# Performance work log

Measured on AMD Instinct MI355X. Metric: run time of the kernel, lower is better.

## Reference

```python
import jax, jax.numpy as jnp
import numpy as np

N_USERS = 100000
N_ITEMS = 50000
D = 64
N_LAYERS = 3
E_RAW = 2_000_000
B = 4096


def setup_inputs() -> dict:
    rng = np.random.RandomState(0)
    u = rng.randint(0, N_USERS, E_RAW).astype(np.int64)
    i = rng.randint(0, N_ITEMS, E_RAW).astype(np.int64)
    lin = np.unique(u * N_ITEMS + i)  # dedupe interactions like the dok_matrix would
    u = (lin // N_ITEMS).astype(np.int32)
    i = (lin % N_ITEMS).astype(np.int32)
    deg_u = np.bincount(u, minlength=N_USERS).astype(np.float64)
    deg_i = np.bincount(i, minlength=N_ITEMS).astype(np.float64)
    inv_u = np.where(deg_u > 0, 1.0 / np.sqrt(np.maximum(deg_u, 1.0)), 0.0)
    inv_i = np.where(deg_i > 0, 1.0 / np.sqrt(np.maximum(deg_i, 1.0)), 0.0)
    val = (inv_u[u] * inv_i[i]).astype(np.float32)  # D^-1/2 A D^-1/2 entries
    # symmetric bipartite Laplacian: user block rows then item block rows
    rows = np.concatenate([u, i + N_USERS]).astype(np.int32)
    cols = np.concatenate([i + N_USERS, u]).astype(np.int32)
    vals = np.concatenate([val, val])

    key = jax.random.key(0)
    k1, k2, k3, k4 = jax.random.split(key, 4)
    embeds = jax.random.normal(k1, (N_USERS + N_ITEMS, D), jnp.float32) * 0.1
    users = jax.random.randint(k2, (B,), 0, N_USERS)
    pos_items = jax.random.randint(k3, (B,), 0, N_ITEMS)
    neg_items = jax.random.randint(k4, (B,), 0, N_ITEMS)
    return dict(embeds=embeds, vals=jnp.asarray(vals), rows=jnp.asarray(rows),
                cols=jnp.asarray(cols), users=users, pos_items=pos_items,
                neg_items=neg_items)


def reference(embeds, vals, rows, cols, users, pos_items, neg_items):
    N = N_USERS + N_ITEMS
    cur = embeds
    acc = embeds  # running sum over layer embeddings (incl. layer 0)
    for _ in range(N_LAYERS):
        msg = vals[:, None] * cur[cols]                      # [nnz, D] gather
        cur = jax.ops.segment_sum(msg, rows, num_segments=N)  # SpMM scatter-add
        acc = acc + cur
    mean = acc / (N_LAYERS + 1)
    user_e = mean[:N_USERS]
    item_e = mean[N_USERS:]
    return user_e[users], item_e[pos_items], item_e[neg_items]
```

## Files before the change

kernel.cpp:

```cpp
#include <hip/hip_runtime.h>
#include <hip/hip_bf16.h>

#define N_USERS 100000
#define N_ITEMS 50000
#define N_TOT   150000
#define D       64
#define NBUCK   ((N_ITEMS + 255) >> 8)
#define BCAP    12288
#define CONVU_B 391
#define FLAG_B  48
#define SCAT_K  32

typedef float v2f __attribute__((ext_vector_type(2)));

__device__ __forceinline__ unsigned bf16rn(float f) {
    unsigned x = __float_as_uint(f);
    return (x + 0x7FFFu + ((x >> 16) & 1u)) >> 16;
}
__device__ __forceinline__ unsigned packbf(float a, float b) {
    return bf16rn(a) | (bf16rn(b) << 16);
}
__device__ __forceinline__ int lower_bound(const int* __restrict__ a, int n, int key) {
    int lo = 0, hi = n;
    while (lo < hi) {
        int mid = (lo + hi) >> 1;
        if (a[mid] < key) lo = mid + 1; else hi = mid;
    }
    return lo;
}

__global__ __launch_bounds__(256) void preA_kernel(
        const float* __restrict__ embeds, const int* __restrict__ rows,
        const int* __restrict__ cols, int* __restrict__ user_ptr,
        unsigned* __restrict__ ebfS, float* __restrict__ invrow,
        const int* __restrict__ users, const int* __restrict__ pos,
        const int* __restrict__ neg, unsigned char* __restrict__ flags,
        int* __restrict__ ccur, int* __restrict__ tmp,
        unsigned short* __restrict__ cols16, int E, int B) {
    int b = blockIdx.x, t = threadIdx.x;
    if (b < CONVU_B) {
        __shared__ int ptr_s[257];
        __shared__ float inv_s[256];
        int base = b * 256;
        int r = base + t;
        int v = lower_bound(rows, E, r);
        ptr_s[t] = v;
        if (r <= N_USERS) user_ptr[r] = v;
        if (t == 0) ptr_s[256] = lower_bound(rows, E, base + 256);
        __syncthreads();
        if (r < N_USERS) {
            int deg = ptr_s[t + 1] - ptr_s[t];
            float inv = (deg > 0) ? (float)(1.0 / sqrt((double)deg)) : 0.f;
            inv_s[t] = inv;
            invrow[r] = inv;
        } else inv_s[t] = 0.f;
        __syncthreads();
        int fl = t & 15;
        #pragma unroll
        for (int i = 0; i < 16; ++i) {
            int lr = i * 16 + (t >> 4);
            int row = base + lr;
            if (row < N_USERS) {
                float inv = inv_s[lr];
                float4 v4 = *(const float4*)(embeds + (size_t)row * D + fl * 4);
                uint2 o;
                o.x = packbf(inv * v4.x, inv * v4.y);
                o.y = packbf(inv * v4.z, inv * v4.w);
                *(uint2*)(ebfS + (size_t)row * 32 + fl * 2) = o;
            }
        }
    } else if (b < CONVU_B + FLAG_B) {
        int k = (b - CONVU_B) * 256 + t;
        if (k < 3 * B) {
            int row;
            if (k < B)          row = users[k];
            else if (k < 2 * B) row = N_USERS + pos[k - B];
            else                row = N_USERS + neg[k - 2 * B];
            flags[row] = 1;
        }
    } else {
        __shared__ int ebuf[256 * SCAT_K];
        __shared__ unsigned char bbuf[256 * SCAT_K];
        __shared__ int cnt[NBUCK];
        __shared__ int basep[NBUCK];
        int chunk = (b - CONVU_B - FLAG_B) * (256 * SCAT_K);
        if (t < NBUCK) cnt[t] = 0;
        __syncthreads();
        #pragma unroll 8
        for (int k = 0; k < SCAT_K; ++k) {
            int e = chunk + k * 256 + t;
            int idx = k * 256 + t;
            if (e < E) {
                int i = cols[e] - N_USERS;
                cols16[e] = (unsigned short)i;
                int bu = i >> 8;
                ebuf[idx] = ((i & 255) << 17) | rows[e];
                bbuf[idx] = (unsigned char)bu;
                atomicAdd(&cnt[bu], 1);
            } else bbuf[idx] = 255;
        }
        __syncthreads();
        if (t < NBUCK) {
            int c = cnt[t];
            basep[t] = c ? atomicAdd(&ccur[t], c) : 0;
            cnt[t] = 0;
        }
        __syncthreads();
        #pragma unroll 4
        for (int k = 0; k < SCAT_K; ++k) {
            int idx = k * 256 + t;
            int bu = bbuf[idx];
            if (bu < NBUCK) {
                int pos2 = basep[bu] + atomicAdd(&cnt[bu], 1);
                if (pos2 < BCAP)
                    tmp[(size_t)bu * BCAP + pos2] = ebuf[idx];
            }
        }
    }
}

__global__ __launch_bounds__(256) void preB_kernel(
        const int* __restrict__ tmp, const int* __restrict__ ccur,
        const float* __restrict__ embeds,
        int* __restrict__ item_beg, int* __restrict__ item_end,
        int* __restrict__ nbr, unsigned* __restrict__ ebfS,
        unsigned* __restrict__ bb1, float* __restrict__ invrow) {
    int b = blockIdx.x, t = threadIdx.x;
    if (b == NBUCK) {
        if (t < 16) {
            *(uint2*)(ebfS + (size_t)N_TOT * 32 + t * 2) = make_uint2(0u, 0u);
            *(uint2*)(bb1  + (size_t)N_TOT * 32 + t * 2) = make_uint2(0u, 0u);
        }
        if (t == 0) invrow[N_TOT] = 0.f;
        return;
    }
    __shared__ int stage[BCAP];
    __shared__ int hist[256];
    __shared__ int scn[256];
    __shared__ int curs[256];
    __shared__ float inv_s[256];
    int n = ccur[b]; if (n > BCAP) n = BCAP;
    const int* src = tmp + (size_t)b * BCAP;
    hist[t] = 0;
    __syncthreads();
    int n4 = n >> 2;
    const int4* src4 = (const int4*)src;
    for (int p = t; p < n4; p += 256) {
        int4 q = src4[p];
        *(int4*)(stage + p * 4) = q;
        atomicAdd(&hist[q.x >> 17], 1);
        atomicAdd(&hist[q.y >> 17], 1);
        atomicAdd(&hist[q.z >> 17], 1);
        atomicAdd(&hist[q.w >> 17], 1);
    }
    for (int p = (n4 << 2) + t; p < n; p += 256) {
        int q = src[p];
        stage[p] = q;
        atomicAdd(&hist[q >> 17], 1);
    }
    __syncthreads();
    scn[t] = hist[t];
    __syncthreads();
    for (int off = 1; off < 256; off <<= 1) {
        int x = (t >= off) ? scn[t - off] : 0;
        __syncthreads();
        scn[t] += x;
        __syncthreads();
    }
    {
        int excl = scn[t] - hist[t];
        curs[t] = excl;
        int gi = (b << 8) + t;
        float inv = (hist[t] > 0) ? (float)(1.0 / sqrt((double)hist[t])) : 0.f;
        inv_s[t] = inv;
        if (gi < N_ITEMS) {
            item_beg[gi] = b * BCAP + excl;
            item_end[gi] = b * BCAP + excl + hist[t];
            invrow[N_USERS + gi] = inv;
        }
    }
    __syncthreads();
    int* dst = nbr + (size_t)b * BCAP;
    for (int p = t; p < n4; p += 256) {
        int4 q = *(const int4*)(stage + p * 4);
        int p0 = atomicAdd(&curs[q.x >> 17], 1); dst[p0] = q.x & 0x1FFFF;
        int p1 = atomicAdd(&curs[q.y >> 17], 1); dst[p1] = q.y & 0x1FFFF;
        int p2 = atomicAdd(&curs[q.z >> 17], 1); dst[p2] = q.z & 0x1FFFF;
        int p3 = atomicAdd(&curs[q.w >> 17], 1); dst[p3] = q.w & 0x1FFFF;
    }
    for (int p = (n4 << 2) + t; p < n; p += 256) {
        int q = stage[p];
        int pos = atomicAdd(&curs[q >> 17], 1);
        dst[pos] = q & 0x1FFFF;
    }
    int fl = t & 15;
    #pragma unroll
    for (int i = 0; i < 16; ++i) {
        int lr = i * 16 + (t >> 4);
        int gi = (b << 8) + lr;
        if (gi < N_ITEMS) {
            int row = N_USERS + gi;
            float inv = inv_s[lr];
            float4 v4 = *(const float4*)(embeds + (size_t)row * D + fl * 4);
            uint2 o;
            o.x = packbf(inv * v4.x, inv * v4.y);
            o.y = packbf(inv * v4.z, inv * v4.w);
            *(uint2*)(ebfS + (size_t)row * 32 + fl * 2) = o;
        }
    }
}

__global__ __launch_bounds__(256) void agg_kernel(
        const unsigned* __restrict__ gsrc,
        float* __restrict__ nxt, unsigned* __restrict__ nxtb,
        const float* __restrict__ invrow,
        const unsigned char* __restrict__ flags,
        const int* __restrict__ user_ptr, const unsigned short* __restrict__ cols16,
        const int* __restrict__ item_beg, const int* __restrict__ item_end,
        const int* __restrict__ nbr) {
    int wave = (int)((blockIdx.x * blockDim.x + threadIdx.x) >> 6);
    int lane = (int)(threadIdx.x & 63);
    if (wave >= (N_TOT >> 2)) return;
    int r  = lane >> 4;
    int q  = lane & 15;
    int g2 = q >> 3;
    int fl = q & 7;

    int row = (wave << 2) + r;
    bool is_user = row < N_USERS;
    int s, epos, dummy;
    const unsigned* sb;
    if (is_user) {
        s = user_ptr[row]; epos = user_ptr[row + 1];
        sb = gsrc + (size_t)N_USERS * 32; dummy = N_ITEMS;
    } else {
        int i = row - N_USERS; s = item_beg[i]; epos = item_end[i];
        sb = gsrc; dummy = N_TOT;
    }
    int deg = epos - s;
    int mdeg = deg;
    mdeg = max(mdeg, __shfl_xor(mdeg, 16));
    mdeg = max(mdeg, __shfl_xor(mdeg, 32));
    int nchunk = (mdeg + 15) >> 4;

    v2f a0 = {0.f, 0.f}, a1 = {0.f, 0.f}, a2 = {0.f, 0.f}, a3 = {0.f, 0.f};

    for (int ch = 0; ch < nchunk; ++ch) {
        int base = s + (ch << 4);
        int cnt = epos - base;
        if (cnt > 16) cnt = 16;
        int col = dummy;
        if (q < cnt)
            col = is_user ? (int)cols16[base + q] : nbr[base + q];
        int cm = mdeg - (ch << 4); if (cm > 16) cm = 16;
        int tcm = (cm + 1) >> 1;
        #pragma unroll 8
        for (int t = 0; t < tcm; ++t) {
            int c = __shfl(col, (r << 4) + 2 * t + g2);
            uint4 qv = *(const uint4*)(sb + (size_t)c * 32 + fl * 4);
            v2f p0 = {__uint_as_float(qv.x << 16), __uint_as_float(qv.x & 0xFFFF0000u)};
            v2f p1 = {__uint_as_float(qv.y << 16), __uint_as_float(qv.y & 0xFFFF0000u)};
            v2f p2 = {__uint_as_float(qv.z << 16), __uint_as_float(qv.z & 0xFFFF0000u)};
            v2f p3 = {__uint_as_float(qv.w << 16), __uint_as_float(qv.w & 0xFFFF0000u)};
            a0 += p0; a1 += p1; a2 += p2; a3 += p3;
        }
    }
    float acc[8] = {a0.x, a0.y, a1.x, a1.y, a2.x, a2.y, a3.x, a3.y};
    #pragma unroll
    for (int j = 0; j < 8; ++j)
        acc[j] += __shfl_xor(acc[j], 8);
    if (q < 8) {
        float inv = invrow[row];
        float f[8];
        #pragma unroll
        for (int j = 0; j < 8; ++j) f[j] = inv * acc[j];
        uint4 o;
        o.x = packbf(inv * f[0], inv * f[1]); o.y = packbf(inv * f[2], inv * f[3]);
        o.z = packbf(inv * f[4], inv * f[5]); o.w = packbf(inv * f[6], inv * f[7]);
        *(uint4*)(nxtb + (size_t)row * 32 + fl * 4) = o;
        if (flags[row]) {
            size_t ro = (size_t)row * D + fl * 8;
            *(float4*)(nxt + ro)     = make_float4(f[0], f[1], f[2], f[3]);
            *(float4*)(nxt + ro + 4) = make_float4(f[4], f[5], f[6], f[7]);
        }
    }
}

__global__ __launch_bounds__(256) void agg3_fused_kernel(
        const unsigned* __restrict__ gsrc,
        const float* __restrict__ e0, const float* __restrict__ e1,
        const float* __restrict__ e2, const float* __restrict__ invrow,
        const int* __restrict__ users, const int* __restrict__ pos,
        const int* __restrict__ neg,
        const int* __restrict__ user_ptr, const unsigned short* __restrict__ cols16,
        const int* __restrict__ item_beg, const int* __restrict__ item_end,
        const int* __restrict__ nbr,
        float* __restrict__ out, int B) {
    int slot = (int)((blockIdx.x * blockDim.x + threadIdx.x) >> 6);
    int lane = (int)(threadIdx.x & 63);
    if (slot >= 3 * B) return;
    int g  = lane >> 3;
    int fl = lane & 7;

    int row;
    if (slot < B)          row = users[slot];
    else if (slot < 2 * B) row = N_USERS + pos[slot - B];
    else                   row = N_USERS + neg[slot - 2 * B];

    bool is_user = row < N_USERS;
    int s, epos, dummy;
    const unsigned* sb;
    if (is_user) {
        s = user_ptr[row]; epos = user_ptr[row + 1];
        sb = gsrc + (size_t)N_USERS * 32; dummy = N_ITEMS;
    } else {
        int i = row - N_USERS; s = item_beg[i]; epos = item_end[i];
        sb = gsrc; dummy = N_TOT;
    }

    v2f a0 = {0.f, 0.f}, a1 = {0.f, 0.f}, a2 = {0.f, 0.f}, a3 = {0.f, 0.f};

    for (int base = s; base < epos; base += 64) {
        int cnt = epos - base; if (cnt > 64) cnt = 64;
        int col = dummy;
        if (lane < cnt)
            col = is_user ? (int)cols16[base + lane] : nbr[base + lane];
        int tcount = (cnt + 7) >> 3;
        #pragma unroll 8
        for (int t = 0; t < tcount; ++t) {
            int c = __shfl(col, 8 * t + g);
            uint4 q = *(const uint4*)(sb + (size_t)c * 32 + fl * 4);
            v2f p0 = {__uint_as_float(q.x << 16), __uint_as_float(q.x & 0xFFFF0000u)};
            v2f p1 = {__uint_as_float(q.y << 16), __uint_as_float(q.y & 0xFFFF0000u)};
            v2f p2 = {__uint_as_float(q.z << 16), __uint_as_float(q.z & 0xFFFF0000u)};
            v2f p3 = {__uint_as_float(q.w << 16), __uint_as_float(q.w & 0xFFFF0000u)};
            a0 += p0; a1 += p1; a2 += p2; a3 += p3;
        }
    }
    float acc[8] = {a0.x, a0.y, a1.x, a1.y, a2.x, a2.y, a3.x, a3.y};
    #pragma unroll
    for (int j = 0; j < 8; ++j) {
        acc[j] += __shfl_xor(acc[j], 8);
        acc[j] += __shfl_xor(acc[j], 16);
        acc[j] += __shfl_xor(acc[j], 32);
    }
    if (lane < 8) {
        float inv = invrow[row];
        size_t ro = (size_t)row * D + fl * 8;
        float4 x0 = *(const float4*)(e0 + ro), x1 = *(const float4*)(e0 + ro + 4);
        float4 y0 = *(const float4*)(e1 + ro), y1 = *(const float4*)(e1 + ro + 4);
        float4 z0 = *(const float4*)(e2 + ro), z1 = *(const float4*)(e2 + ro + 4);
        float4 r0, r1;
        r0.x = (x0.x + y0.x + z0.x + inv * acc[0]) * 0.25f;
        r0.y = (x0.y + y0.y + z0.y + inv * acc[1]) * 0.25f;
        r0.z = (x0.z + y0.z + z0.z + inv * acc[2]) * 0.25f;
        r0.w = (x0.w + y0.w + z0.w + inv * acc[3]) * 0.25f;
        r1.x = (x1.x + y1.x + z1.x + inv * acc[4]) * 0.25f;
        r1.y = (x1.y + y1.y + z1.y + inv * acc[5]) * 0.25f;
        r1.z = (x1.z + y1.z + z1.z + inv * acc[6]) * 0.25f;
        r1.w = (x1.w + y1.w + z1.w + inv * acc[7]) * 0.25f;
        size_t oo = (size_t)slot * D + fl * 8;
        *(float4*)(out + oo)     = r0;
        *(float4*)(out + oo + 4) = r1;
    }
}

extern "C" void kernel_launch(void* const* d_in, const int* in_sizes, int n_in,
                              void* d_out, int out_size, void* d_ws, size_t ws_size,
                              hipStream_t stream) {
    const float* embeds = (const float*)d_in[0];
    const int*   rows   = (const int*)d_in[2];
    const int*   cols   = (const int*)d_in[3];
    const int*   users  = (const int*)d_in[4];
    const int*   pos    = (const int*)d_in[5];
    const int*   neg    = (const int*)d_in[6];
    const int E2 = in_sizes[1];
    const int E  = E2 / 2;
    const int B  = in_sizes[4];

    char* ws = (char*)d_ws;
    size_t off = 0;
    auto alloc = [&](size_t bytes) { void* p = ws + off; off = (off + bytes + 255) & ~(size_t)255; return p; };
    float*    buf1     = (float*)   alloc((size_t)N_TOT * D * sizeof(float));
    float*    buf2     = (float*)   alloc((size_t)N_TOT * D * sizeof(float));
    unsigned* ebfS     = (unsigned*)alloc((size_t)(N_TOT + 1) * 32 * sizeof(unsigned));
    unsigned* bb1      = (unsigned*)alloc((size_t)(N_TOT + 1) * 32 * sizeof(unsigned));
    int*      nbr      = (int*)     alloc((size_t)NBUCK * BCAP * sizeof(int));
    unsigned short* cols16 = (unsigned short*)alloc((size_t)E * sizeof(unsigned short));
    int*      user_ptr = (int*)     alloc((size_t)(N_USERS + 1) * sizeof(int));
    int*      item_beg = (int*)     alloc((size_t)N_ITEMS * sizeof(int));
    int*      item_end = (int*)     alloc((size_t)N_ITEMS * sizeof(int));
    float*    invrow   = (float*)   alloc((size_t)(N_TOT + 1) * sizeof(float));
    int*      ccur     = (int*)     alloc((size_t)NBUCK * sizeof(int));
    unsigned char* flags = (unsigned char*)alloc((size_t)N_TOT);
    int*      tmp      = (int*)buf1;

    size_t zspan = ((char*)flags + N_TOT) - (char*)ccur;
    hipMemsetAsync(ccur, 0, zspan, stream);
    const int scatB = (E + 256 * SCAT_K - 1) / (256 * SCAT_K);
    preA_kernel<<<CONVU_B + FLAG_B + scatB, 256, 0, stream>>>(
        embeds, rows, cols, user_ptr, ebfS, invrow, users, pos, neg, flags,
        ccur, tmp, cols16, E, B);
    preB_kernel<<<NBUCK + 1, 256, 0, stream>>>(
        tmp, ccur, embeds, item_beg, item_end, nbr, ebfS, bb1, invrow);

    const int blocks = N_TOT / 16;
    agg_kernel<<<blocks, 256, 0, stream>>>(ebfS, buf1, bb1, invrow, flags, user_ptr,
                                           cols16, item_beg, item_end, nbr);
    agg_kernel<<<blocks, 256, 0, stream>>>(bb1, buf2, ebfS, invrow, flags, user_ptr,
                                           cols16, item_beg, item_end, nbr);

    agg3_fused_kernel<<<(3 * B + 3) / 4, 256, 0, stream>>>(
        ebfS, embeds, buf1, buf2, invrow, users, pos, neg,
        user_ptr, cols16, item_beg, item_end, nbr, (float*)d_out, B);
}
```

Baseline: 292.6 us.

## Build user CSR pointers from row boundaries during scatter instead of binary search

Replaces the per-user binary search over the sorted rows array with boundary detection in the edge-scatter pass: each edge compares its row with the next and writes user_ptr for the users in between. The user-degree normalisation and bf16 conversion of user embeddings move into extra blocks of the second preprocessing kernel, which now reads the finished user_ptr. This removes about 100k log(E) dependent global-memory searches, at the cost of an extra adjacent load per edge and loop-based pointer writes.

```diff
diff --git a/kernel.cpp b/kernel.cpp
--- a/kernel.cpp
+++ b/kernel.cpp
@@ -20,57 +20,17 @@
 __device__ __forceinline__ unsigned packbf(float a, float b) {
     return bf16rn(a) | (bf16rn(b) << 16);
 }
-__device__ __forceinline__ int lower_bound(const int* __restrict__ a, int n, int key) {
-    int lo = 0, hi = n;
-    while (lo < hi) {
-        int mid = (lo + hi) >> 1;
-        if (a[mid] < key) lo = mid + 1; else hi = mid;
-    }
-    return lo;
-}
 
 __global__ __launch_bounds__(256) void preA_kernel(
-        const float* __restrict__ embeds, const int* __restrict__ rows,
-        const int* __restrict__ cols, int* __restrict__ user_ptr,
-        unsigned* __restrict__ ebfS, float* __restrict__ invrow,
-        const int* __restrict__ users, const int* __restrict__ pos,
-        const int* __restrict__ neg, unsigned char* __restrict__ flags,
+        const int* __restrict__ rows, const int* __restrict__ cols,
+        int* __restrict__ user_ptr, const int* __restrict__ users,
+        const int* __restrict__ pos, const int* __restrict__ neg,
+        unsigned char* __restrict__ flags,
         int* __restrict__ ccur, int* __restrict__ tmp,
         unsigned short* __restrict__ cols16, int E, int B) {
     int b = blockIdx.x, t = threadIdx.x;
-    if (b < CONVU_B) {
-        __shared__ int ptr_s[257];
-        __shared__ float inv_s[256];
-        int base = b * 256;
-        int r = base + t;
-        int v = lower_bound(rows, E, r);
-        ptr_s[t] = v;
-        if (r <= N_USERS) user_ptr[r] = v;
-        if (t == 0) ptr_s[256] = lower_bound(rows, E, base + 256);
-        __syncthreads();
-        if (r < N_USERS) {
-            int deg = ptr_s[t + 1] - ptr_s[t];
-            float inv = (deg > 0) ? (float)(1.0 / sqrt((double)deg)) : 0.f;
-            inv_s[t] = inv;
-            invrow[r] = inv;
-        } else inv_s[t] = 0.f;
-        __syncthreads();
-        int fl = t & 15;
-        #pragma unroll
-        for (int i = 0; i < 16; ++i) {
-            int lr = i * 16 + (t >> 4);
-            int row = base + lr;
-            if (row < N_USERS) {
-                float inv = inv_s[lr];
-                float4 v4 = *(const float4*)(embeds + (size_t)row * D + fl * 4);
-                uint2 o;
-                o.x = packbf(inv * v4.x, inv * v4.y);
-                o.y = packbf(inv * v4.z, inv * v4.w);
-                *(uint2*)(ebfS + (size_t)row * 32 + fl * 2) = o;
-            }
-        }
-    } else if (b < CONVU_B + FLAG_B) {
-        int k = (b - CONVU_B) * 256 + t;
+    if (b < FLAG_B) {
+        int k = b * 256 + t;
         if (k < 3 * B) {
             int row;
             if (k < B)          row = users[k];
@@ -83,7 +43,7 @@
         __shared__ unsigned char bbuf[256 * SCAT_K];
         __shared__ int cnt[NBUCK];
         __shared__ int basep[NBUCK];
-        int chunk = (b - CONVU_B - FLAG_B) * (256 * SCAT_K);
+        int chunk = (b - FLAG_B) * (256 * SCAT_K);
         if (t < NBUCK) cnt[t] = 0;
         __syncthreads();
         #pragma unroll 8
@@ -91,12 +51,17 @@
             int e = chunk + k * 256 + t;
             int idx = k * 256 + t;
             if (e < E) {
-                int i = cols[e] - N_USERS;
+                int i  = cols[e] - N_USERS;
+                int rv = rows[e];
                 cols16[e] = (unsigned short)i;
                 int bu = i >> 8;
-                ebuf[idx] = ((i & 255) << 17) | rows[e];
+                ebuf[idx] = ((i & 255) << 17) | rv;
                 bbuf[idx] = (unsigned char)bu;
                 atomicAdd(&cnt[bu], 1);
+                int rn = (e + 1 < E) ? rows[e + 1] : N_USERS;
+                for (int u = rv + 1; u <= rn; ++u) user_ptr[u] = e + 1;
+                if (e == 0)
+                    for (int u = 0; u <= rv; ++u) user_ptr[u] = 0;
             } else bbuf[idx] = 255;
         }
         __syncthreads();
@@ -121,24 +86,55 @@
 
 __global__ __launch_bounds__(256) void preB_kernel(
         const int* __restrict__ tmp, const int* __restrict__ ccur,
-        const float* __restrict__ embeds,
+        const float* __restrict__ embeds, const int* __restrict__ user_ptr,
         int* __restrict__ item_beg, int* __restrict__ item_end,
         int* __restrict__ nbr, unsigned* __restrict__ ebfS,
-        unsigned* __restrict__ bb1, float* __restrict__ invrow) {
+        unsigned* __restrict__ bb1, float* __restrict__ invrow, int E) {
     int b = blockIdx.x, t = threadIdx.x;
-    if (b == NBUCK) {
-        if (t < 16) {
-            *(uint2*)(ebfS + (size_t)N_TOT * 32 + t * 2) = make_uint2(0u, 0u);
-            *(uint2*)(bb1  + (size_t)N_TOT * 32 + t * 2) = make_uint2(0u, 0u);
-        }
-        if (t == 0) invrow[N_TOT] = 0.f;
-        return;
-    }
     __shared__ int stage[BCAP];
     __shared__ int hist[256];
     __shared__ int scn[256];
     __shared__ int curs[256];
     __shared__ float inv_s[256];
+    if (b == NBUCK) {
+        if (t < 16) {
+            *(uint2*)(ebfS + (size_t)N_TOT * 32 + t * 2) = make_uint2(0u, 0u);
+            *(uint2*)(bb1  + (size_t)N_TOT * 32 + t * 2) = make_uint2(0u, 0u);
+        }
+        if (t == 0) invrow[N_TOT] = 0.f;
+        return;
+    }
+    if (b > NBUCK) {
+        int base = (b - NBUCK - 1) * 256;
+        int r = base + t;
+        int* ptr_s = stage;
+        ptr_s[t] = (r <= N_USERS) ? user_ptr[r] : E;
+        if (t == 0) ptr_s[256] = (base + 256 <= N_USERS) ? user_ptr[base + 256] : E;
+        __syncthreads();
+        float inv = 0.f;
+        if (r < N_USERS) {
+            int deg = ptr_s[t + 1] - ptr_s[t];
+            inv = (deg > 0) ? (float)(1.0 / sqrt((double)deg)) : 0.f;
+            invrow[r] = inv;
+        }
+        inv_s[t] = inv;
+        __syncthreads();
+        int fl = t & 15;
+        #pragma unroll
+        for (int i = 0; i < 16; ++i) {
+            int lr = i * 16 + (t >> 4);
+            int row = base + lr;
+            if (row < N_USERS) {
+                float iv = inv_s[lr];
+                float4 v4 = *(const float4*)(embeds + (size_t)row * D + fl * 4);
+                uint2 o;
+                o.x = packbf(iv * v4.x, iv * v4.y);
+                o.y = packbf(iv * v4.z, iv * v4.w);
+                *(uint2*)(ebfS + (size_t)row * 32 + fl * 2) = o;
+            }
+        }
+        return;
+    }
     int n = ccur[b]; if (n > BCAP) n = BCAP;
     const int* src = tmp + (size_t)b * BCAP;
     hist[t] = 0;
@@ -398,11 +394,10 @@
     size_t zspan = ((char*)flags + N_TOT) - (char*)ccur;
     hipMemsetAsync(ccur, 0, zspan, stream);
     const int scatB = (E + 256 * SCAT_K - 1) / (256 * SCAT_K);
-    preA_kernel<<<CONVU_B + FLAG_B + scatB, 256, 0, stream>>>(
-        embeds, rows, cols, user_ptr, ebfS, invrow, users, pos, neg, flags,
-        ccur, tmp, cols16, E, B);
-    preB_kernel<<<NBUCK + 1, 256, 0, stream>>>(
-        tmp, ccur, embeds, item_beg, item_end, nbr, ebfS, bb1, invrow);
+    preA_kernel<<<FLAG_B + scatB, 256, 0, stream>>>(
+        rows, cols, user_ptr, users, pos, neg, flags, ccur, tmp, cols16, E, B);
+    preB_kernel<<<NBUCK + 1 + CONVU_B, 256, 0, stream>>>(
+        tmp, ccur, embeds, user_ptr, item_beg, item_end, nbr, ebfS, bb1, invrow, E);
 
     const int blocks = N_TOT / 16;
     agg_kernel<<<blocks, 256, 0, stream>>>(ebfS, buf1, bb1, invrow, flags, user_ptr,
```

Measured after the change: 302.3 us. 1.03x slower.

## Sort aggregation rows by degree to balance per-wave work

Applied to the files above, without the earlier changes.

Builds a degree histogram during preprocessing, then adds a counting-sort kernel that writes a degree-ordered row permutation. The aggregation kernels read their rows through that permutation, so the four rows sharing a wave have similar degree. This is meant to cut idle lanes, since each wave loops to the maximum degree of its rows. In exchange it adds a kernel launch, heavily contended global atomics on a few histogram bins, and scattered row order, which can hurt gather and store locality.

```diff
diff --git a/kernel.cpp b/kernel.cpp
--- a/kernel.cpp
+++ b/kernel.cpp
@@ -10,6 +10,7 @@
 #define CONVU_B 391
 #define FLAG_B  48
 #define SCAT_K  32
+#define PERM_B  ((N_TOT + 255) >> 8)
 
 typedef float v2f __attribute__((ext_vector_type(2)));
 
@@ -36,7 +37,8 @@
         const int* __restrict__ users, const int* __restrict__ pos,
         const int* __restrict__ neg, unsigned char* __restrict__ flags,
         int* __restrict__ ccur, int* __restrict__ tmp,
-        unsigned short* __restrict__ cols16, int E, int B) {
+        unsigned short* __restrict__ cols16, int* __restrict__ gbins,
+        int E, int B) {
     int b = blockIdx.x, t = threadIdx.x;
     if (b < CONVU_B) {
         __shared__ int ptr_s[257];
@@ -53,6 +55,7 @@
             float inv = (deg > 0) ? (float)(1.0 / sqrt((double)deg)) : 0.f;
             inv_s[t] = inv;
             invrow[r] = inv;
+            atomicAdd(&gbins[min(deg, 255)], 1);
         } else inv_s[t] = 0.f;
         __syncthreads();
         int fl = t & 15;
@@ -124,7 +127,8 @@
         const float* __restrict__ embeds,
         int* __restrict__ item_beg, int* __restrict__ item_end,
         int* __restrict__ nbr, unsigned* __restrict__ ebfS,
-        unsigned* __restrict__ bb1, float* __restrict__ invrow) {
+        unsigned* __restrict__ bb1, float* __restrict__ invrow,
+        int* __restrict__ gbins) {
     int b = blockIdx.x, t = threadIdx.x;
     if (b == NBUCK) {
         if (t < 16) {
@@ -177,6 +181,7 @@
             item_beg[gi] = b * BCAP + excl;
             item_end[gi] = b * BCAP + excl + hist[t];
             invrow[N_USERS + gi] = inv;
+            atomicAdd(&gbins[min(hist[t], 255)], 1);
         }
     }
     __syncthreads();
@@ -210,6 +215,32 @@
     }
 }
 
+__global__ __launch_bounds__(256) void preC_kernel(
+        const int* __restrict__ user_ptr, const int* __restrict__ item_beg,
+        const int* __restrict__ item_end, const int* __restrict__ gbins,
+        int* __restrict__ gcur, int* __restrict__ perm) {
+    __shared__ int pre[256];
+    int t = threadIdx.x;
+    int row = blockIdx.x * 256 + t;
+    pre[t] = gbins[t];
+    __syncthreads();
+    for (int off = 1; off < 256; off <<= 1) {
+        int x = (t >= off) ? pre[t - off] : 0;
+        __syncthreads();
+        pre[t] += x;
+        __syncthreads();
+    }
+    if (row < N_TOT) {
+        int deg;
+        if (row < N_USERS) deg = user_ptr[row + 1] - user_ptr[row];
+        else { int i = row - N_USERS; deg = item_end[i] - item_beg[i]; }
+        int bin = min(deg, 255);
+        int excl = pre[bin] - gbins[bin];
+        int pos = excl + atomicAdd(&gcur[bin], 1);
+        perm[pos] = row;
+    }
+}
+
 __global__ __launch_bounds__(256) void agg_kernel(
         const unsigned* __restrict__ gsrc,
         float* __restrict__ nxt, unsigned* __restrict__ nxtb,
@@ -217,7 +248,7 @@
         const unsigned char* __restrict__ flags,
         const int* __restrict__ user_ptr, const unsigned short* __restrict__ cols16,
         const int* __restrict__ item_beg, const int* __restrict__ item_end,
-        const int* __restrict__ nbr) {
+        const int* __restrict__ nbr, const int* __restrict__ perm) {
     int wave = (int)((blockIdx.x * blockDim.x + threadIdx.x) >> 6);
     int lane = (int)(threadIdx.x & 63);
     if (wave >= (N_TOT >> 2)) return;
@@ -226,7 +257,7 @@
     int g2 = q >> 3;
     int fl = q & 7;
 
-    int row = (wave << 2) + r;
+    int row = perm[(wave << 2) + r];
     bool is_user = row < N_USERS;
     int s, epos, dummy;
     const unsigned* sb;
@@ -391,7 +422,10 @@
     int*      item_beg = (int*)     alloc((size_t)N_ITEMS * sizeof(int));
     int*      item_end = (int*)     alloc((size_t)N_ITEMS * sizeof(int));
     float*    invrow   = (float*)   alloc((size_t)(N_TOT + 1) * sizeof(float));
+    int*      perm     = (int*)     alloc((size_t)N_TOT * sizeof(int));
     int*      ccur     = (int*)     alloc((size_t)NBUCK * sizeof(int));
+    int*      gbins    = (int*)     alloc(256 * sizeof(int));
+    int*      gcur     = (int*)     alloc(256 * sizeof(int));
     unsigned char* flags = (unsigned char*)alloc((size_t)N_TOT);
     int*      tmp      = (int*)buf1;
 
@@ -400,15 +434,17 @@
     const int scatB = (E + 256 * SCAT_K - 1) / (256 * SCAT_K);
     preA_kernel<<<CONVU_B + FLAG_B + scatB, 256, 0, stream>>>(
         embeds, rows, cols, user_ptr, ebfS, invrow, users, pos, neg, flags,
-        ccur, tmp, cols16, E, B);
+        ccur, tmp, cols16, gbins, E, B);
     preB_kernel<<<NBUCK + 1, 256, 0, stream>>>(
-        tmp, ccur, embeds, item_beg, item_end, nbr, ebfS, bb1, invrow);
+        tmp, ccur, embeds, item_beg, item_end, nbr, ebfS, bb1, invrow, gbins);
+    preC_kernel<<<PERM_B, 256, 0, stream>>>(
+        user_ptr, item_beg, item_end, gbins, gcur, perm);
 
     const int blocks = N_TOT / 16;
     agg_kernel<<<blocks, 256, 0, stream>>>(ebfS, buf1, bb1, invrow, flags, user_ptr,
-                                           cols16, item_beg, item_end, nbr);
+                                           cols16, item_beg, item_end, nbr, perm);
     agg_kernel<<<blocks, 256, 0, stream>>>(bb1, buf2, ebfS, invrow, flags, user_ptr,
-                                           cols16, item_beg, item_end, nbr);
+                                           cols16, item_beg, item_end, nbr, perm);
 
     agg3_fused_kernel<<<(3 * B + 3) / 4, 256, 0, stream>>>(
         ebfS, embeds, buf1, buf2, invrow, users, pos, neg,
```

Result: slower. 1.014 ms (+246.4%).
